# Kernel optimization log

Measured on AMD Instinct MI355X. Metric: run time of the kernel, lower is better.

The kernel has to match this reference:

```python
import jax, jax.numpy as jnp
import numpy as np

N_NODES = 50000
N_EDGES = 1600000
IN_CH = 512
OUT_CH = 48


def setup_inputs() -> dict:
    key = jax.random.key(0)
    k1, k2, k3, k4 = jax.random.split(key, 4)
    edge_index = jax.random.randint(k1, (2, N_EDGES), 0, N_NODES, dtype=jnp.int64)
    features = jax.random.normal(k2, (N_NODES, IN_CH), dtype=jnp.float32)
    edge_weights = jax.random.uniform(k3, (N_EDGES,), dtype=jnp.float32)
    # glorot-initialized weight, zero bias (as in reset_parameters)
    stdv = float(np.sqrt(6.0 / (IN_CH + OUT_CH)))
    weight = jax.random.uniform(k4, (IN_CH, OUT_CH), dtype=jnp.float32,
                                minval=-stdv, maxval=stdv)
    bias = jnp.zeros((OUT_CH,), dtype=jnp.float32)
    return {"edge_index": edge_index, "features": features,
            "edge_weights": edge_weights, "weight": weight, "bias": bias}


def reference(edge_index, features, edge_weights, weight, bias):
    # dense projection: [N, in] @ [in, out] -> [N, out]
    xw = jnp.matmul(features, weight)
    src, dst = edge_index[0], edge_index[1]
    # message: norm * x_j, gathered from source nodes  -> [E, out]
    msgs = edge_weights[:, None] * xw[src]
    # aggregate (add) at target nodes -> [N, out]
    aggr = jax.ops.segment_sum(msgs, dst, num_segments=N_NODES)
    z = aggr + bias
    return jax.nn.log_softmax(z, axis=1)
```

## Files before the change

kernel.cpp:

```cpp
#include <hip/hip_runtime.h>
#include <math.h>

#define N_NODES 50000
#define N_EDGES 1600000
#define IN_CH   512
#define OUT_CH  48
#define XW_LD   64
#define N_TILES (N_NODES / 16)

#define BSHIFT  6
#define BNODES  64
#define NB      ((N_NODES + BNODES - 1) / BNODES)
#define ETILE   4096
#define CAP     2816
#define CHUNK   128

#define BFRAG_SHORTS (16 * 3 * 64 * 8)

#define PREP_BLOCKS 24
#define HIST_BLOCKS 256
#define GEMMB_BLOCKS ((N_TILES + 7) / 8)
#define BIN_BLOCKS   ((N_EDGES + ETILE - 1) / ETILE)

typedef __attribute__((ext_vector_type(8))) short bf16x8;
typedef __attribute__((ext_vector_type(4))) float f32x4;

static __device__ inline short f2bf(float x) {
    union { float f; unsigned u; } in; in.f = x;
    unsigned r = in.u + 0x7fffu + ((in.u >> 16) & 1u);
    return (short)(r >> 16);
}
static __device__ inline float bf2f(unsigned v16) {
    union { unsigned u; float f; } o; o.u = v16 << 16; return o.f;
}

static __device__ void prep_body(const float* __restrict__ w,
                                 unsigned short* __restrict__ wfrag) {
    int i = blockIdx.x * 256 + threadIdx.x;
    if (i >= IN_CH * OUT_CH / 4) return;
    int flat = i * 4;
    int k   = flat / OUT_CH;
    int col = flat % OUT_CH;
    float4 v = *reinterpret_cast<const float4*>(w + flat);
    int s = k >> 5, j = k & 7, q = (k >> 3) & 3;
    float vv[4] = {v.x, v.y, v.z, v.w};
    #pragma unroll
    for (int c = 0; c < 4; ++c) {
        int cc = col + c;
        int t  = cc >> 4;
        int ln = (cc & 15) | (q << 4);
        wfrag[((s * 3 + t) * 64 + ln) * 8 + j] = (unsigned short)f2bf(vv[c]);
    }
}

__global__ __launch_bounds__(256) void prep_hist(const float* __restrict__ w,
                                                 unsigned short* __restrict__ wfrag,
                                                 const int* __restrict__ dst,
                                                 int* __restrict__ counts) {
    __shared__ int hc[NB];
    if (blockIdx.x < PREP_BLOCKS) { prep_body(w, wfrag); return; }
    int bid = blockIdx.x - PREP_BLOCKS;
    for (int i = threadIdx.x; i < NB; i += 256) hc[i] = 0;
    __syncthreads();
    for (int e = bid * 256 + threadIdx.x; e < N_EDGES; e += HIST_BLOCKS * 256)
        atomicAdd(&hc[dst[e] >> BSHIFT], 1);
    __syncthreads();
    for (int i = threadIdx.x; i < NB; i += 256)
        if (hc[i]) atomicAdd(&counts[i], hc[i]);
}

__global__ __launch_bounds__(1024) void bucket_scan(const int* __restrict__ counts,
                                                    int* __restrict__ base,
                                                    int* __restrict__ cursor) {
    __shared__ int sdata[1024];
    int t = threadIdx.x;
    int i0 = 2 * t, i1 = 2 * t + 1;
    int v0 = (i0 < NB) ? counts[i0] : 0;
    int v1 = (i1 < NB) ? counts[i1] : 0;
    int s = v0 + v1;
    sdata[t] = s;
    __syncthreads();
    for (int d = 1; d < 1024; d <<= 1) {
        int x = (t >= d) ? sdata[t - d] : 0;
        __syncthreads();
        sdata[t] += x;
        __syncthreads();
    }
    int excl = sdata[t] - s;
    if (i0 < NB) { base[i0] = excl;      cursor[i0] = excl; }
    if (i1 < NB) { base[i1] = excl + v0; cursor[i1] = excl + v0; }
}

static __device__ void gemm_body512(char* smem, const float* __restrict__ f,
                                    const unsigned short* __restrict__ wfrag,
                                    unsigned short* __restrict__ xw) {
    short* sBl = reinterpret_cast<short*>(smem);

    int tid  = threadIdx.x;
    int lane = tid & 63;
    int wid  = tid >> 6;

    {
        const uint4* gw = reinterpret_cast<const uint4*>(wfrag);
        uint4*       sw = reinterpret_cast<uint4*>(smem);
        #pragma unroll
        for (int i = 0; i < BFRAG_SHORTS / 8 / 512; ++i)
            sw[i * 512 + tid] = gw[i * 512 + tid];
    }
    __syncthreads();

    int tile = blockIdx.x * 8 + wid;
    if (tile >= N_TILES) return;

    const bf16x8* sB = reinterpret_cast<const bf16x8*>(sBl);

    int row = tile * 16 + (lane & 15);
    const float* fp = f + (size_t)row * IN_CH + ((lane >> 4) << 3);

    f32x4 acc0 = {0.f, 0.f, 0.f, 0.f};
    f32x4 acc1 = {0.f, 0.f, 0.f, 0.f};
    f32x4 acc2 = {0.f, 0.f, 0.f, 0.f};

    float4 a0[2], a1[2];
    a0[0] = *reinterpret_cast<const float4*>(fp);
    a1[0] = *reinterpret_cast<const float4*>(fp + 4);

    #pragma unroll
    for (int s = 0; s < 16; ++s) {
        const int cb = s & 1, nb = cb ^ 1;
        if (s + 1 < 16) {
            a0[nb] = *reinterpret_cast<const float4*>(fp + (s + 1) * 32);
            a1[nb] = *reinterpret_cast<const float4*>(fp + (s + 1) * 32 + 4);
        }
        bf16x8 a;
        a[0] = f2bf(a0[cb].x); a[1] = f2bf(a0[cb].y);
        a[2] = f2bf(a0[cb].z); a[3] = f2bf(a0[cb].w);
        a[4] = f2bf(a1[cb].x); a[5] = f2bf(a1[cb].y);
        a[6] = f2bf(a1[cb].z); a[7] = f2bf(a1[cb].w);
        bf16x8 b0 = sB[(s * 3 + 0) * 64 + lane];
        bf16x8 b1 = sB[(s * 3 + 1) * 64 + lane];
        bf16x8 b2 = sB[(s * 3 + 2) * 64 + lane];
        acc0 = __builtin_amdgcn_mfma_f32_16x16x32_bf16(a, b0, acc0, 0, 0, 0);
        acc1 = __builtin_amdgcn_mfma_f32_16x16x32_bf16(a, b1, acc1, 0, 0, 0);
        acc2 = __builtin_amdgcn_mfma_f32_16x16x32_bf16(a, b2, acc2, 0, 0, 0);
    }

    unsigned short* orow = xw + (size_t)tile * 16 * XW_LD;
    int c  = lane & 15;
    int r0 = (lane >> 4) * 4;
    #pragma unroll
    for (int r = 0; r < 4; ++r) {
        orow[(size_t)(r0 + r) * XW_LD +  0 + c] = (unsigned short)f2bf(acc0[r]);
        orow[(size_t)(r0 + r) * XW_LD + 16 + c] = (unsigned short)f2bf(acc1[r]);
        orow[(size_t)(r0 + r) * XW_LD + 32 + c] = (unsigned short)f2bf(acc2[r]);
    }
}

static __device__ void bin_body(char* smem, int bid, const int* __restrict__ src,
                                const int* __restrict__ dst, const float* __restrict__ ew,
                                int* __restrict__ cursor, int2* __restrict__ epack) {
    int*   hist  = reinterpret_cast<int*>(smem);
    int*   loff  = reinterpret_cast<int*>(smem + 3200);
    int*   gbase = reinterpret_cast<int*>(smem + 6400);
    int*   ssum  = reinterpret_cast<int*>(smem + 9600);
    int2*  buf   = reinterpret_cast<int2*>(smem + 11648);
    short* bkt   = reinterpret_cast<short*>(smem + 44416);

    int tid = threadIdx.x;
    int tileStart = bid * ETILE;
    int tileN = N_EDGES - tileStart; if (tileN > ETILE) tileN = ETILE;

    for (int i = tid; i < NB; i += 512) hist[i] = 0;
    __syncthreads();

    int rank[ETILE / 512];
    int dreg[ETILE / 512];
    #pragma unroll
    for (int k = 0; k < ETILE / 512; ++k) {
        int e = tileStart + k * 512 + tid;
        dreg[k] = (e < N_EDGES) ? dst[e] : 0;
        rank[k] = (e < N_EDGES) ? atomicAdd(&hist[dreg[k] >> BSHIFT], 1) : 0;
    }
    __syncthreads();

    for (int i = tid; i < NB; i += 512) {
        int c = hist[i];
        gbase[i] = c ? atomicAdd(&cursor[i], c) : 0;
    }

    int a0 = (2 * tid     < NB) ? hist[2 * tid]     : 0;
    int a1 = (2 * tid + 1 < NB) ? hist[2 * tid + 1] : 0;
    ssum[tid] = a0 + a1;
    __syncthreads();
    for (int d = 1; d < 512; d <<= 1) {
        int x = (tid >= d) ? ssum[tid - d] : 0;
        __syncthreads();
        ssum[tid] += x;
        __syncthreads();
    }
    int excl = ssum[tid] - (a0 + a1);
    if (2 * tid     < NB) loff[2 * tid]     = excl;
    if (2 * tid + 1 < NB) loff[2 * tid + 1] = excl + a0;
    __syncthreads();

    #pragma unroll
    for (int k = 0; k < ETILE / 512; ++k) {
        int e = tileStart + k * 512 + tid;
        if (e < N_EDGES) {
            int d = dreg[k];
            int b = d >> BSHIFT;
            int slot = loff[b] + rank[k];
            int2 p;
            p.x = (src[e] & 0xFFFF) | (d << 16);
            p.y = __float_as_int(ew[e]);
            buf[slot] = p;
            bkt[slot] = (short)b;
        }
    }
    __syncthreads();

    for (int idx = tid; idx < tileN; idx += 512) {
        int b = bkt[idx];
        epack[gbase[b] + idx - loff[b]] = buf[idx];
    }
}

__global__ __launch_bounds__(512) void gemm_bin(const float* __restrict__ f,
                                                const unsigned short* __restrict__ wfrag,
                                                unsigned short* __restrict__ xw,
                                                const int* __restrict__ src,
                                                const int* __restrict__ dst,
                                                const float* __restrict__ ew,
                                                int* __restrict__ cursor,
                                                int2* __restrict__ epack) {
    __shared__ __align__(16) char smem[52608];
    if (blockIdx.x < GEMMB_BLOCKS) gemm_body512(smem, f, wfrag, xw);
    else bin_body(smem, blockIdx.x - GEMMB_BLOCKS, src, dst, ew, cursor, epack);
}

__global__ __launch_bounds__(512) void sort_bucket(const int* __restrict__ base,
                                                   const int* __restrict__ cursor,
                                                   int2* __restrict__ epack) {
    __shared__ int2  A[CAP];
    __shared__ int2  B[CAP];
    __shared__ short rk[CAP];
    __shared__ int   hist[BNODES];
    __shared__ int   loff[BNODES];

    int b  = blockIdx.x;
    int lo = base[b], hi = cursor[b];
    int len = hi - lo;
    if (len <= 0 || len > CAP) return;

    int tid = threadIdx.x;
    if (tid < BNODES) hist[tid] = 0;
    for (int i = tid; i < len; i += 512) A[i] = epack[lo + i];
    __syncthreads();

    for (int i = tid; i < len; i += 512) {
        int key = (((unsigned)A[i].x) >> 16) & (BNODES - 1);
        rk[i] = (short)atomicAdd(&hist[key], 1);
    }
    __syncthreads();

    if (tid < BNODES) {
        int v = hist[tid];
        int s = v;
        #pragma unroll
        for (int d = 1; d < 64; d <<= 1) {
            int t = __shfl_up(s, d);
            if (tid >= d) s += t;
        }
        loff[tid] = s - v;
    }
    __syncthreads();

    for (int i = tid; i < len; i += 512) {
        int key = (((unsigned)A[i].x) >> 16) & (BNODES - 1);
        B[loff[key] + rk[i]] = A[i];
    }
    __syncthreads();

    for (int i = tid; i < len; i += 512) epack[lo + i] = B[i];
}

__global__ __launch_bounds__(512) void seg_aggregate(const int2* __restrict__ epack,
                                                     const unsigned short* __restrict__ xw,
                                                     float* __restrict__ out) {
    int wv   = (blockIdx.x * blockDim.x + threadIdx.x) >> 6;
    int lane = threadIdx.x & 63;
    int base = wv * CHUNK;
    if (base >= N_EDGES) return;
    int h  = lane >> 5;
    int cp = lane & 31;
    bool act = (cp < 24);

    int2 E0 = epack[base + lane];
    int2 E1 = epack[base + 64 + lane];

    float ax = 0.f, ay = 0.f;
    int cur = ((unsigned)__shfl(E0.x, h)) >> 16;

    int px[2][8]; float pw[2][8]; unsigned u[2][8];

    #pragma unroll
    for (int k = 0; k < 8; ++k) {
        int idx = ((2 * k) & 63) | h;
        px[0][k] = __shfl(E0.x, idx);
        pw[0][k] = __int_as_float(__shfl(E0.y, idx));
    }
    #pragma unroll
    for (int k = 0; k < 8; ++k)
        u[0][k] = *reinterpret_cast<const unsigned*>(
            xw + (size_t)(px[0][k] & 0xFFFF) * XW_LD + (cp << 1));

    #pragma unroll
    for (int j = 0; j < 8; ++j) {
        const int cb = j & 1, nb = cb ^ 1;
        if (j + 1 < 8) {
            #pragma unroll
            for (int k = 0; k < 8; ++k) {
                int t  = (j + 1) * 8 + k;
                int sx = (t < 32) ? E0.x : E1.x;
                int sy = (t < 32) ? E0.y : E1.y;
                int idx = ((2 * t) & 63) | h;
                px[nb][k] = __shfl(sx, idx);
                pw[nb][k] = __int_as_float(__shfl(sy, idx));
            }
            #pragma unroll
            for (int k = 0; k < 8; ++k)
                u[nb][k] = *reinterpret_cast<const unsigned*>(
                    xw + (size_t)(px[nb][k] & 0xFFFF) * XW_LD + (cp << 1));
        }
        #pragma unroll
        for (int k = 0; k < 8; ++k) {
            int node = ((unsigned)px[cb][k]) >> 16;
            if (node != cur) {
                if (act) {
                    atomicAdd(&out[(size_t)cur * OUT_CH + cp     ], ax);
                    atomicAdd(&out[(size_t)cur * OUT_CH + 24 + cp], ay);
                }
                ax = 0.f; ay = 0.f; cur = node;
            }
            float    wf = pw[cb][k];
            unsigned uu = u[cb][k];
            ax = fmaf(wf, bf2f(uu & 0xFFFFu), ax);
            ay = fmaf(wf, bf2f(uu >> 16), ay);
        }
    }

    if (act) {
        atomicAdd(&out[(size_t)cur * OUT_CH + cp     ], ax);
        atomicAdd(&out[(size_t)cur * OUT_CH + 24 + cp], ay);
    }
}

__global__ __launch_bounds__(256) void lsm_rows(float* __restrict__ z,
                                                const float* __restrict__ bias) {
    int node = (blockIdx.x * blockDim.x + threadIdx.x) >> 6;
    int lane = threadIdx.x & 63;
    if (node >= N_NODES) return;
    bool ch = (lane < OUT_CH);

    int pos = (lane >> 1) + 24 * (lane & 1);
    float v = ch ? (z[(size_t)node * OUT_CH + pos] + bias[lane]) : -INFINITY;
    float m = v;
    #pragma unroll
    for (int d = 32; d >= 1; d >>= 1) m = fmaxf(m, __shfl_xor(m, d));
    float e = ch ? expf(v - m) : 0.f;
    float s = e;
    #pragma unroll
    for (int d = 32; d >= 1; d >>= 1) s += __shfl_xor(s, d);
    float lse = m + logf(s);
    __syncthreads();
    if (ch) z[(size_t)node * OUT_CH + lane] = v - lse;
}

extern "C" void kernel_launch(void* const* d_in, const int* in_sizes, int n_in,
                              void* d_out, int out_size, void* d_ws, size_t ws_size,
                              hipStream_t stream) {
    const int*   edge_index = (const int*)d_in[0];
    const float* features   = (const float*)d_in[1];
    const float* eweights   = (const float*)d_in[2];
    const float* weight     = (const float*)d_in[3];
    const float* bias       = (const float*)d_in[4];

    const int* src = edge_index;
    const int* dst = edge_index + N_EDGES;

    float* out = (float*)d_out;

    char* ws = (char*)d_ws;
    unsigned short* xw    = (unsigned short*)(ws + 0);
    int*   counts = (int*)  (ws + 9600000);
    int*   base   = (int*)  (ws + 9616000);
    int*   cursor = (int*)  (ws + 9632000);
    int2*  epack  = (int2*) (ws + 9648000);
    unsigned short* wfrag = (unsigned short*)(ws + 22448000);

    hipMemsetAsync(counts, 0, NB * sizeof(int), stream);
    hipMemsetAsync(d_out, 0, (size_t)N_NODES * OUT_CH * sizeof(float), stream);

    prep_hist<<<PREP_BLOCKS + HIST_BLOCKS, 256, 0, stream>>>(weight, wfrag, dst, counts);

    bucket_scan<<<1, 1024, 0, stream>>>(counts, base, cursor);
    gemm_bin<<<GEMMB_BLOCKS + BIN_BLOCKS, 512, 0, stream>>>(features, wfrag, xw,
                                                            src, dst, eweights,
                                                            cursor, epack);

    sort_bucket<<<NB, 512, 0, stream>>>(base, cursor, epack);

    {
        int nWaves  = N_EDGES / CHUNK;
        int nBlocks = (nWaves + 7) / 8;
        seg_aggregate<<<nBlocks, 512, 0, stream>>>(epack, xw, out);
    }
    lsm_rows<<<(N_NODES + 3) / 4, 256, 0, stream>>>(out, bias);
}
```

Before: 127.9 us.

## Shrink fused gemm/bin LDS footprint to raise occupancy

Halves the edge tile per binning block, drops the separate bucket-id LDS array by recomputing the bucket from the packed dst bits, and makes the GEMM read weight fragments directly from global memory instead of staging them in LDS. Together these cut the fused kernel's shared memory from about 52KB to about 28KB so more blocks can be resident per CU. The trade-offs are twice as many binning blocks with more per-block histogram/scan overhead, and repeated global/L2 reads of the weight fragments in the GEMM path.

```diff
diff --git a/kernel.cpp b/kernel.cpp
--- a/kernel.cpp
+++ b/kernel.cpp
@@ -11,7 +11,7 @@
 #define BSHIFT  6
 #define BNODES  64
 #define NB      ((N_NODES + BNODES - 1) / BNODES)
-#define ETILE   4096
+#define ETILE   2048
 #define CAP     2816
 #define CHUNK   128
 
@@ -21,6 +21,8 @@
 #define HIST_BLOCKS 256
 #define GEMMB_BLOCKS ((N_TILES + 7) / 8)
 #define BIN_BLOCKS   ((N_EDGES + ETILE - 1) / ETILE)
+
+#define BIN_SMEM 28032
 
 typedef __attribute__((ext_vector_type(8))) short bf16x8;
 typedef __attribute__((ext_vector_type(4))) float f32x4;
@@ -91,28 +93,17 @@
     if (i1 < NB) { base[i1] = excl + v0; cursor[i1] = excl + v0; }
 }
 
-static __device__ void gemm_body512(char* smem, const float* __restrict__ f,
+static __device__ void gemm_body512(const float* __restrict__ f,
                                     const unsigned short* __restrict__ wfrag,
                                     unsigned short* __restrict__ xw) {
-    short* sBl = reinterpret_cast<short*>(smem);
-
     int tid  = threadIdx.x;
     int lane = tid & 63;
     int wid  = tid >> 6;
 
-    {
-        const uint4* gw = reinterpret_cast<const uint4*>(wfrag);
-        uint4*       sw = reinterpret_cast<uint4*>(smem);
-        #pragma unroll
-        for (int i = 0; i < BFRAG_SHORTS / 8 / 512; ++i)
-            sw[i * 512 + tid] = gw[i * 512 + tid];
-    }
-    __syncthreads();
-
     int tile = blockIdx.x * 8 + wid;
     if (tile >= N_TILES) return;
 
-    const bf16x8* sB = reinterpret_cast<const bf16x8*>(sBl);
+    const bf16x8* gB = reinterpret_cast<const bf16x8*>(wfrag);
 
     int row = tile * 16 + (lane & 15);
     const float* fp = f + (size_t)row * IN_CH + ((lane >> 4) << 3);
@@ -137,9 +128,9 @@
         a[2] = f2bf(a0[cb].z); a[3] = f2bf(a0[cb].w);
         a[4] = f2bf(a1[cb].x); a[5] = f2bf(a1[cb].y);
         a[6] = f2bf(a1[cb].z); a[7] = f2bf(a1[cb].w);
-        bf16x8 b0 = sB[(s * 3 + 0) * 64 + lane];
-        bf16x8 b1 = sB[(s * 3 + 1) * 64 + lane];
-        bf16x8 b2 = sB[(s * 3 + 2) * 64 + lane];
+        bf16x8 b0 = gB[(s * 3 + 0) * 64 + lane];
+        bf16x8 b1 = gB[(s * 3 + 1) * 64 + lane];
+        bf16x8 b2 = gB[(s * 3 + 2) * 64 + lane];
         acc0 = __builtin_amdgcn_mfma_f32_16x16x32_bf16(a, b0, acc0, 0, 0, 0);
         acc1 = __builtin_amdgcn_mfma_f32_16x16x32_bf16(a, b1, acc1, 0, 0, 0);
         acc2 = __builtin_amdgcn_mfma_f32_16x16x32_bf16(a, b2, acc2, 0, 0, 0);
@@ -159,12 +150,11 @@
 static __device__ void bin_body(char* smem, int bid, const int* __restrict__ src,
                                 const int* __restrict__ dst, const float* __restrict__ ew,
                                 int* __restrict__ cursor, int2* __restrict__ epack) {
-    int*   hist  = reinterpret_cast<int*>(smem);
-    int*   loff  = reinterpret_cast<int*>(smem + 3200);
-    int*   gbase = reinterpret_cast<int*>(smem + 6400);
-    int*   ssum  = reinterpret_cast<int*>(smem + 9600);
-    int2*  buf   = reinterpret_cast<int2*>(smem + 11648);
-    short* bkt   = reinterpret_cast<short*>(smem + 44416);
+    int*  hist  = reinterpret_cast<int*>(smem);
+    int*  loff  = reinterpret_cast<int*>(smem + 3200);
+    int*  gbase = reinterpret_cast<int*>(smem + 6400);
+    int*  ssum  = reinterpret_cast<int*>(smem + 9600);
+    int2* buf   = reinterpret_cast<int2*>(smem + 11648);
 
     int tid = threadIdx.x;
     int tileStart = bid * ETILE;
@@ -214,14 +204,14 @@
             p.x = (src[e] & 0xFFFF) | (d << 16);
             p.y = __float_as_int(ew[e]);
             buf[slot] = p;
-            bkt[slot] = (short)b;
         }
     }
     __syncthreads();
 
     for (int idx = tid; idx < tileN; idx += 512) {
-        int b = bkt[idx];
-        epack[gbase[b] + idx - loff[b]] = buf[idx];
+        int2 p = buf[idx];
+        int b = (int)(((unsigned)p.x) >> (16 + BSHIFT));
+        epack[gbase[b] + idx - loff[b]] = p;
     }
 }
 
@@ -233,8 +223,8 @@
                                                 const float* __restrict__ ew,
                                                 int* __restrict__ cursor,
                                                 int2* __restrict__ epack) {
-    __shared__ __align__(16) char smem[52608];
-    if (blockIdx.x < GEMMB_BLOCKS) gemm_body512(smem, f, wfrag, xw);
+    __shared__ __align__(16) char smem[BIN_SMEM];
+    if (blockIdx.x < GEMMB_BLOCKS) gemm_body512(f, wfrag, xw);
     else bin_body(smem, blockIdx.x - GEMMB_BLOCKS, src, dst, ew, cursor, epack);
 }
 
```

Measured after the change: 135.5 us. 6.0% more time.
